# Kernel optimization log

Measured on AMD Instinct MI355X. Metric: run time of the kernel, lower is better.

The kernel has to match this reference:

```python
import jax, jax.numpy as jnp
import numpy as np

GRID_SIZE = 5
SPLINE_ORDER = 3
HIDDEN = 128
N = 131072
K = 256          # num_cluster
EPS = 1e-8       # torch.cosine_similarity eps
N_COEF = GRID_SIZE + SPLINE_ORDER  # 8 spline basis functions per input feature


def make_grid():
    # efficient-kan grid: grid_range [-1,1], extended by spline_order on each side
    h = 2.0 / GRID_SIZE
    g = jnp.arange(-SPLINE_ORDER, GRID_SIZE + SPLINE_ORDER + 1, dtype=jnp.float32) * h - 1.0
    return jnp.tile(g[None, :], (HIDDEN, 1))  # (in, grid_size + 2*order + 1) = (128, 12)


def b_splines(x, grid):
    # x: (N, in), grid: (in, G) -> bases: (N, in, grid_size + spline_order)
    xe = x[..., None]
    bases = ((xe >= grid[:, :-1]) & (xe < grid[:, 1:])).astype(x.dtype)
    for p in range(1, SPLINE_ORDER + 1):
        left = (xe - grid[:, :-(p + 1)]) / (grid[:, p:-1] - grid[:, :-(p + 1)])
        right = (grid[:, p + 1:] - xe) / (grid[:, p + 1:] - grid[:, 1:-p])
        bases = left * bases[..., :-1] + right * bases[..., 1:]
    return bases


def kan_linear(x, grid, base_w, spline_w, scaler):
    # efficient-kan KANLinear: base path + spline path
    base = jax.nn.silu(x) @ base_w.T                       # (N, out)
    sp = b_splines(x, grid)                                # (N, in, coef)
    sw = spline_w * scaler[..., None]                      # (out, in, coef)
    return base + jnp.einsum('nic,oic->no', sp, sw)


def setup_inputs() -> dict:
    key = jax.random.key(0)
    ks = jax.random.split(key, 9)
    s = 1.0 / np.sqrt(HIDDEN)
    return {
        'x': jax.random.normal(ks[0], (N, HIDDEN), jnp.float32),
        'prototypes': jax.random.normal(ks[1], (K, HIDDEN), jnp.float32),
        'grid': make_grid(),
        'base_w1': jax.random.normal(ks[2], (HIDDEN, HIDDEN), jnp.float32) * s,
        'spline_w1': jax.random.normal(ks[3], (HIDDEN, HIDDEN, N_COEF), jnp.float32) * 0.1,
        'scaler1': jax.random.normal(ks[4], (HIDDEN, HIDDEN), jnp.float32) * s + 1.0,
        'base_w2': jax.random.normal(ks[5], (HIDDEN, HIDDEN), jnp.float32) * s,
        'spline_w2': jax.random.normal(ks[6], (HIDDEN, HIDDEN, N_COEF), jnp.float32) * 0.1,
        'scaler2': jax.random.normal(ks[7], (HIDDEN, HIDDEN), jnp.float32) * s + 1.0,
    }


def reference(x, prototypes, grid, base_w1, spline_w1, scaler1, base_w2, spline_w2, scaler2):
    # KAN([128,128,128]) = two KANLinear layers
    h = kan_linear(x, grid, base_w1, spline_w1, scaler1)
    emb = kan_linear(h, grid, base_w2, spline_w2, scaler2)     # (N, 128)
    # cosine similarity to all prototypes = normalized matmul (same math as
    # the broadcasted torch.cosine_similarity, without the (N,K,H) intermediate)
    xn = emb / jnp.maximum(jnp.linalg.norm(emb, axis=-1, keepdims=True), EPS)
    pn = prototypes / jnp.maximum(jnp.linalg.norm(prototypes, axis=-1, keepdims=True), EPS)
    sim = xn @ pn.T                                            # (N, K)
    cluster_assignments = jnp.argmax(sim, axis=1)              # (N,)
    return emb, cluster_assignments
```

## Files before the change

### kernel.cpp

```cpp
#include <hip/hip_runtime.h>
#include <math.h>

typedef unsigned short u16;
typedef _Float16 f16;
typedef __attribute__((ext_vector_type(8))) _Float16 f16x8;
typedef __attribute__((ext_vector_type(2))) _Float16 f16x2;
typedef __attribute__((ext_vector_type(4))) float f32x4;

#define N_ROWS 131072
#define HID 128
#define WS_CH 8192
#define N_WCH 72
#define N_PCH 8

__device__ __forceinline__ void split8(const float* a8, f16x8& hv, f16x8& lv) {
    union { f16x8 v; f16x2 p[4]; } H, L;
    #pragma unroll
    for (int j = 0; j < 4; ++j) {
        float v0 = a8[2 * j], v1 = a8[2 * j + 1];
        float h0 = __builtin_bit_cast(float, __builtin_bit_cast(unsigned, v0) & 0xFFFFE000u);
        float h1 = __builtin_bit_cast(float, __builtin_bit_cast(unsigned, v1) & 0xFFFFE000u);
        H.p[j] = __builtin_bit_cast(f16x2, __builtin_amdgcn_cvt_pkrtz(v0, v1));
        L.p[j] = __builtin_bit_cast(f16x2, __builtin_amdgcn_cvt_pkrtz(v0 - h0, v1 - h1));
    }
    hv = H.v; lv = L.v;
}

__device__ __forceinline__ void spline8(float xv, float* a8) {
    float s  = (xv + 2.2f) * 2.5f;
    float tf = floorf(s);
    int   tt = (int)tf;
    bool valid = (tt >= 0) && (tt <= 10);
    float kt = (float)(tt - 3) * 0.4f - 1.0f;
    float u  = (xv - kt) * 2.5f;
    float u2 = u * u, u3 = u2 * u;
    float om = 1.0f - u;
    float b3 = u3 * (1.0f / 6.0f);
    float b2 = (-3.f * u3 + 3.f * u2 + 3.f * u + 1.f) * (1.0f / 6.0f);
    float b1 = (3.f * u3 - 6.f * u2 + 4.f) * (1.0f / 6.0f);
    float b0 = om * om * om * (1.0f / 6.0f);
    #pragma unroll
    for (int c = 0; c < 8; ++c) {
        int d = tt - c;
        float v = 0.f;
        v = (d == 0) ? b3 : v;
        v = (d == 1) ? b2 : v;
        v = (d == 2) ? b1 : v;
        v = (d == 3) ? b0 : v;
        a8[c] = valid ? v : 0.f;
    }
}

__device__ __forceinline__ int tswz(int r, int c) {
    return (r << 7) + ((((c >> 2) ^ r) & 31) << 2) + (c & 3);
}

__global__ __launch_bounds__(256)
void pack_weights(const float* __restrict__ bw1, const float* __restrict__ sw1,
                  const float* __restrict__ sc1,
                  const float* __restrict__ bw2, const float* __restrict__ sw2,
                  const float* __restrict__ sc2,
                  const float* __restrict__ protos, u16* __restrict__ ws)
{
    int gid = blockIdx.x * 256 + threadIdx.x;
    if (gid < N_WCH * 4096) {
        int l  = gid / (36 * 4096);
        int r  = gid % (36 * 4096);
        int ch = r / 4096;
        int e  = r % 4096;
        int o  = e >> 5;
        int kl = e & 31;
        const float* bw = l ? bw2 : bw1;
        const float* sw = l ? sw2 : sw1;
        const float* sc = l ? sc2 : sc1;
        float v;
        if (ch < 4) {
            v = bw[o * HID + ch * 32 + kl];
        } else {
            int i = (ch - 4) * 4 + (kl >> 3);
            v = sw[(o * HID + i) * 8 + (kl & 7)] * sc[o * HID + i];
        }
        f16 hi = (f16)v;
        f16 lo = (f16)(v - (float)hi);
        int nt = o >> 4, n = o & 15, kq = kl >> 3, c = kl & 7;
        size_t base = (size_t)(l * 36 + ch) * WS_CH;
        size_t idx  = ((size_t)nt * 64 + kq * 16 + n) * 8 + c;
        ws[base + idx]        = __builtin_bit_cast(u16, hi);
        ws[base + 4096 + idx] = __builtin_bit_cast(u16, lo);
    } else if (gid < (N_WCH + N_PCH) * 4096) {
        int r  = gid - N_WCH * 4096;
        int hk = r / 4096;
        int e  = r % 4096;
        int pl = e >> 5;
        int kl = e & 31;
        int half = hk >> 2, kc = hk & 3;
        int p = half * 128 + pl;
        const float4 pv = *(const float4*)(protos + (size_t)p * HID + kl * 4);
        float s = pv.x * pv.x + pv.y * pv.y + pv.z * pv.z + pv.w * pv.w;
        #pragma unroll
        for (int off = 1; off < 32; off <<= 1) s += __shfl_xor(s, off);
        float rp = 1.0f / fmaxf(sqrtf(s), 1e-8f);
        float v = protos[(size_t)p * HID + kc * 32 + kl] * rp;
        f16 hi = (f16)v;
        f16 lo = (f16)(v - (float)hi);
        int nt = pl >> 4, n = pl & 15, kq = kl >> 3, c = kl & 7;
        size_t base = (size_t)(N_WCH + hk) * WS_CH;
        size_t idx  = ((size_t)nt * 64 + kq * 16 + n) * 8 + c;
        ws[base + idx]        = __builtin_bit_cast(u16, hi);
        ws[base + 4096 + idx] = __builtin_bit_cast(u16, lo);
    }
}

__global__ __launch_bounds__(256, 3)
void kan_fused(const float* __restrict__ x, const u16* __restrict__ wpack,
               float* __restrict__ emb_out, float* __restrict__ assign_out)
{
    __shared__ float t[64 * 128];
    __shared__ u16   Bfrag[2][8][64][8];

    const int tid  = threadIdx.x;
    const int lane = tid & 63;
    const int w    = tid >> 6;
    const int m    = lane & 15;
    const int q    = lane >> 4;
    const int row  = w * 16 + m;
    const int brow = blockIdx.x * 64;

    const char* gptr = (const char*)wpack + (size_t)w * 4096 + (size_t)lane * 16;
    uint4* const lptr = (uint4*)&Bfrag[0][0][0][0] + w * 256 + lane;
    uint4 rr0, rr1, rr2, rr3;

#define ISSUE_LOADS() do {                                                         \
        rr0 = *(const uint4*)(gptr);                                               \
        rr1 = *(const uint4*)(gptr + 1024);                                        \
        rr2 = *(const uint4*)(gptr + 2048);                                        \
        rr3 = *(const uint4*)(gptr + 3072);                                        \
        gptr += 16384;                                                             \
    } while (0)

#define STORE_LDS() do {                                                           \
        lptr[0] = rr0; lptr[64] = rr1; lptr[128] = rr2; lptr[192] = rr3;           \
    } while (0)

#define PIPE_BARRIER() do {                                                        \
        asm volatile("s_waitcnt lgkmcnt(0)" ::: "memory");                         \
        __builtin_amdgcn_s_barrier();                                              \
        __builtin_amdgcn_sched_barrier(0);                                         \
    } while (0)

    ISSUE_LOADS();

    {
        const int m2 = tid >> 2, kq2 = tid & 3;
        const float4* src = (const float4*)(x + (size_t)(brow + m2) * HID + kq2 * 32);
        #pragma unroll
        for (int j = 0; j < 8; ++j) {
            float4 v = src[j];
            *(float4*)&t[tswz(m2, kq2 * 32 + j * 4)] = v;
        }
    }

    f16x8 ahv, alv, bhv, blv;
    f32x4 acc[8];

    for (int l = 0; l < 2; ++l) {
        #pragma unroll
        for (int nt = 0; nt < 8; ++nt) acc[nt] = (f32x4){0.f, 0.f, 0.f, 0.f};

        for (int ch = 0; ch < 36; ++ch) {
            float a8[8];
            if (ch < 4) {
                float4 v0 = *(const float4*)&t[tswz(row, ch * 32 + q * 8)];
                float4 v1 = *(const float4*)&t[tswz(row, ch * 32 + q * 8 + 4)];
                float xs[8] = {v0.x, v0.y, v0.z, v0.w, v1.x, v1.y, v1.z, v1.w};
                #pragma unroll
                for (int j = 0; j < 8; ++j)
                    a8[j] = xs[j] * __builtin_amdgcn_rcpf(1.0f + __expf(-xs[j]));
            } else {
                spline8(t[tswz(row, (ch - 4) * 4 + q)], a8);
            }
            split8(a8, ahv, alv);

            PIPE_BARRIER();
            STORE_LDS();
            ISSUE_LOADS();
            PIPE_BARRIER();

            __builtin_amdgcn_s_setprio(1);
            #pragma unroll
            for (int nt = 0; nt < 8; ++nt) {
                bhv = *(const f16x8*)Bfrag[0][nt][lane];
                blv = *(const f16x8*)Bfrag[1][nt][lane];
                acc[nt] = __builtin_amdgcn_mfma_f32_16x16x32_f16(ahv, bhv, acc[nt], 0, 0, 0);
                acc[nt] = __builtin_amdgcn_mfma_f32_16x16x32_f16(alv, bhv, acc[nt], 0, 0, 0);
                acc[nt] = __builtin_amdgcn_mfma_f32_16x16x32_f16(ahv, blv, acc[nt], 0, 0, 0);
            }
            __builtin_amdgcn_s_setprio(0);
        }

        #pragma unroll
        for (int nt = 0; nt < 8; ++nt)
            #pragma unroll
            for (int r = 0; r < 4; ++r)
                t[tswz(w * 16 + q * 4 + r, nt * 16 + m)] = acc[nt][r];
    }

    {
        const int m2 = tid >> 2, kq2 = tid & 3;
        float* dst = emb_out + (size_t)(brow + m2) * HID + kq2 * 32;
        #pragma unroll
        for (int j = 0; j < 8; ++j)
            *(float4*)(dst + j * 4) = *(const float4*)&t[tswz(m2, kq2 * 32 + j * 4)];
    }

    float best[4]; int bi[4];
    #pragma unroll
    for (int r = 0; r < 4; ++r) { best[r] = -3.402823466e+38f; bi[r] = 0; }

    for (int half = 0; half < 2; ++half) {
        #pragma unroll
        for (int nt = 0; nt < 8; ++nt) acc[nt] = (f32x4){0.f, 0.f, 0.f, 0.f};

        for (int kc = 0; kc < 4; ++kc) {
            const int reg = N_WCH + half * 4 + kc;

            float a8[8];
            {
                float4 v0 = *(const float4*)&t[tswz(row, kc * 32 + q * 8)];
                float4 v1 = *(const float4*)&t[tswz(row, kc * 32 + q * 8 + 4)];
                a8[0] = v0.x; a8[1] = v0.y; a8[2] = v0.z; a8[3] = v0.w;
                a8[4] = v1.x; a8[5] = v1.y; a8[6] = v1.z; a8[7] = v1.w;
            }
            split8(a8, ahv, alv);

            PIPE_BARRIER();
            STORE_LDS();
            if (reg != 79) ISSUE_LOADS();
            PIPE_BARRIER();

            __builtin_amdgcn_s_setprio(1);
            #pragma unroll
            for (int nt = 0; nt < 8; ++nt) {
                bhv = *(const f16x8*)Bfrag[0][nt][lane];
                blv = *(const f16x8*)Bfrag[1][nt][lane];
                acc[nt] = __builtin_amdgcn_mfma_f32_16x16x32_f16(ahv, bhv, acc[nt], 0, 0, 0);
                acc[nt] = __builtin_amdgcn_mfma_f32_16x16x32_f16(alv, bhv, acc[nt], 0, 0, 0);
                acc[nt] = __builtin_amdgcn_mfma_f32_16x16x32_f16(ahv, blv, acc[nt], 0, 0, 0);
            }
            __builtin_amdgcn_s_setprio(0);
        }

        #pragma unroll
        for (int nt = 0; nt < 8; ++nt) {
            int p = half * 128 + nt * 16 + m;
            #pragma unroll
            for (int r = 0; r < 4; ++r) {
                float v = acc[nt][r];
                if (v > best[r]) { best[r] = v; bi[r] = p; }
            }
        }
    }

    #pragma unroll
    for (int r = 0; r < 4; ++r) {
        #pragma unroll
        for (int off = 1; off < 16; off <<= 1) {
            float ov = __shfl_xor(best[r], off);
            int   oi = __shfl_xor(bi[r], off);
            if (ov > best[r] || (ov == best[r] && oi < bi[r])) { best[r] = ov; bi[r] = oi; }
        }
        if (m == 0)
            assign_out[(size_t)brow + w * 16 + q * 4 + r] = (float)bi[r];
    }
#undef ISSUE_LOADS
#undef STORE_LDS
#undef PIPE_BARRIER
}

extern "C" void kernel_launch(void* const* d_in, const int* in_sizes, int n_in,
                              void* d_out, int out_size, void* d_ws, size_t ws_size,
                              hipStream_t stream) {
    (void)in_sizes; (void)n_in; (void)out_size; (void)ws_size;

    const float* x      = (const float*)d_in[0];
    const float* protos = (const float*)d_in[1];
    const float* bw1 = (const float*)d_in[3];
    const float* sw1 = (const float*)d_in[4];
    const float* sc1 = (const float*)d_in[5];
    const float* bw2 = (const float*)d_in[6];
    const float* sw2 = (const float*)d_in[7];
    const float* sc2 = (const float*)d_in[8];

    float* out    = (float*)d_out;
    float* embp   = out;
    float* assign = out + (size_t)N_ROWS * HID;
    u16*   wpack  = (u16*)d_ws;

    pack_weights<<<dim3((N_WCH + N_PCH) * 4096 / 256), dim3(256), 0, stream>>>(
        bw1, sw1, sc1, bw2, sw2, sc2, protos, wpack);
    kan_fused<<<dim3(N_ROWS / 64), dim3(256), 0, stream>>>(
        x, wpack, embp, assign);
}
```

Measured before the change: 398.2 us.

## Process two 16-row M-tiles per wave to double B-fragment reuse

Each block now handles 128 rows instead of 64, and each wave computes two 16-row tiles that share the same staged B fragments from LDS. This halves the per-row cost of weight streaming, LDS B reads and barrier overhead. In exchange the block uses a larger LDS tile (64KB for t) and twice the accumulator registers, and launch bounds drop to 2 blocks per CU, so occupancy falls and latency hiding is reduced.

```diff
diff --git a/kernel.cpp b/kernel.cpp
--- a/kernel.cpp
+++ b/kernel.cpp
@@ -111,11 +111,11 @@
     }
 }
 
-__global__ __launch_bounds__(256, 3)
+__global__ __launch_bounds__(256, 2)
 void kan_fused(const float* __restrict__ x, const u16* __restrict__ wpack,
                float* __restrict__ emb_out, float* __restrict__ assign_out)
 {
-    __shared__ float t[64 * 128];
+    __shared__ float t[128 * 128];
     __shared__ u16   Bfrag[2][8][64][8];
 
     const int tid  = threadIdx.x;
@@ -123,8 +123,8 @@
     const int w    = tid >> 6;
     const int m    = lane & 15;
     const int q    = lane >> 4;
-    const int row  = w * 16 + m;
-    const int brow = blockIdx.x * 64;
+    const int row0 = w * 32 + m;
+    const int brow = blockIdx.x * 128;
 
     const char* gptr = (const char*)wpack + (size_t)w * 4096 + (size_t)lane * 16;
     uint4* const lptr = (uint4*)&Bfrag[0][0][0][0] + w * 256 + lane;
@@ -151,35 +151,45 @@
     ISSUE_LOADS();
 
     {
-        const int m2 = tid >> 2, kq2 = tid & 3;
-        const float4* src = (const float4*)(x + (size_t)(brow + m2) * HID + kq2 * 32);
-        #pragma unroll
-        for (int j = 0; j < 8; ++j) {
+        const int m2 = tid >> 1, hf = tid & 1;
+        const float4* src = (const float4*)(x + (size_t)(brow + m2) * HID + hf * 64);
+        #pragma unroll
+        for (int j = 0; j < 16; ++j) {
             float4 v = src[j];
-            *(float4*)&t[tswz(m2, kq2 * 32 + j * 4)] = v;
-        }
-    }
-
-    f16x8 ahv, alv, bhv, blv;
-    f32x4 acc[8];
+            *(float4*)&t[tswz(m2, hf * 64 + j * 4)] = v;
+        }
+    }
+
+    f16x8 ah0, al0, ah1, al1, bhv, blv;
+    f32x4 acc0[8], acc1[8];
 
     for (int l = 0; l < 2; ++l) {
         #pragma unroll
-        for (int nt = 0; nt < 8; ++nt) acc[nt] = (f32x4){0.f, 0.f, 0.f, 0.f};
+        for (int nt = 0; nt < 8; ++nt) {
+            acc0[nt] = (f32x4){0.f, 0.f, 0.f, 0.f};
+            acc1[nt] = (f32x4){0.f, 0.f, 0.f, 0.f};
+        }
 
         for (int ch = 0; ch < 36; ++ch) {
-            float a8[8];
+            float a80[8], a81[8];
             if (ch < 4) {
-                float4 v0 = *(const float4*)&t[tswz(row, ch * 32 + q * 8)];
-                float4 v1 = *(const float4*)&t[tswz(row, ch * 32 + q * 8 + 4)];
-                float xs[8] = {v0.x, v0.y, v0.z, v0.w, v1.x, v1.y, v1.z, v1.w};
+                float4 u0 = *(const float4*)&t[tswz(row0, ch * 32 + q * 8)];
+                float4 u1 = *(const float4*)&t[tswz(row0, ch * 32 + q * 8 + 4)];
+                float4 v0 = *(const float4*)&t[tswz(row0 + 16, ch * 32 + q * 8)];
+                float4 v1 = *(const float4*)&t[tswz(row0 + 16, ch * 32 + q * 8 + 4)];
+                float xs0[8] = {u0.x, u0.y, u0.z, u0.w, u1.x, u1.y, u1.z, u1.w};
+                float xs1[8] = {v0.x, v0.y, v0.z, v0.w, v1.x, v1.y, v1.z, v1.w};
                 #pragma unroll
-                for (int j = 0; j < 8; ++j)
-                    a8[j] = xs[j] * __builtin_amdgcn_rcpf(1.0f + __expf(-xs[j]));
+                for (int j = 0; j < 8; ++j) {
+                    a80[j] = xs0[j] * __builtin_amdgcn_rcpf(1.0f + __expf(-xs0[j]));
+                    a81[j] = xs1[j] * __builtin_amdgcn_rcpf(1.0f + __expf(-xs1[j]));
+                }
             } else {
-                spline8(t[tswz(row, (ch - 4) * 4 + q)], a8);
-            }
-            split8(a8, ahv, alv);
+                spline8(t[tswz(row0,      (ch - 4) * 4 + q)], a80);
+                spline8(t[tswz(row0 + 16, (ch - 4) * 4 + q)], a81);
+            }
+            split8(a80, ah0, al0);
+            split8(a81, ah1, al1);
 
             PIPE_BARRIER();
             STORE_LDS();
@@ -191,9 +201,12 @@
             for (int nt = 0; nt < 8; ++nt) {
                 bhv = *(const f16x8*)Bfrag[0][nt][lane];
                 blv = *(const f16x8*)Bfrag[1][nt][lane];
-                acc[nt] = __builtin_amdgcn_mfma_f32_16x16x32_f16(ahv, bhv, acc[nt], 0, 0, 0);
-                acc[nt] = __builtin_amdgcn_mfma_f32_16x16x32_f16(alv, bhv, acc[nt], 0, 0, 0);
-                acc[nt] = __builtin_amdgcn_mfma_f32_16x16x32_f16(ahv, blv, acc[nt], 0, 0, 0);
+                acc0[nt] = __builtin_amdgcn_mfma_f32_16x16x32_f16(ah0, bhv, acc0[nt], 0, 0, 0);
+                acc0[nt] = __builtin_amdgcn_mfma_f32_16x16x32_f16(al0, bhv, acc0[nt], 0, 0, 0);
+                acc0[nt] = __builtin_amdgcn_mfma_f32_16x16x32_f16(ah0, blv, acc0[nt], 0, 0, 0);
+                acc1[nt] = __builtin_amdgcn_mfma_f32_16x16x32_f16(ah1, bhv, acc1[nt], 0, 0, 0);
+                acc1[nt] = __builtin_amdgcn_mfma_f32_16x16x32_f16(al1, bhv, acc1[nt], 0, 0, 0);
+                acc1[nt] = __builtin_amdgcn_mfma_f32_16x16x32_f16(ah1, blv, acc1[nt], 0, 0, 0);
             }
             __builtin_amdgcn_s_setprio(0);
         }
@@ -201,37 +214,50 @@
         #pragma unroll
         for (int nt = 0; nt < 8; ++nt)
             #pragma unroll
-            for (int r = 0; r < 4; ++r)
-                t[tswz(w * 16 + q * 4 + r, nt * 16 + m)] = acc[nt][r];
+            for (int r = 0; r < 4; ++r) {
+                t[tswz(w * 32 + q * 4 + r,      nt * 16 + m)] = acc0[nt][r];
+                t[tswz(w * 32 + 16 + q * 4 + r, nt * 16 + m)] = acc1[nt][r];
+            }
     }
 
     {
-        const int m2 = tid >> 2, kq2 = tid & 3;
-        float* dst = emb_out + (size_t)(brow + m2) * HID + kq2 * 32;
-        #pragma unroll
-        for (int j = 0; j < 8; ++j)
-            *(float4*)(dst + j * 4) = *(const float4*)&t[tswz(m2, kq2 * 32 + j * 4)];
-    }
-
-    float best[4]; int bi[4];
+        const int m2 = tid >> 1, hf = tid & 1;
+        float* dst = emb_out + (size_t)(brow + m2) * HID + hf * 64;
+        #pragma unroll
+        for (int j = 0; j < 16; ++j)
+            *(float4*)(dst + j * 4) = *(const float4*)&t[tswz(m2, hf * 64 + j * 4)];
+    }
+
+    float best0[4], best1[4]; int bi0[4], bi1[4];
     #pragma unroll
-    for (int r = 0; r < 4; ++r) { best[r] = -3.402823466e+38f; bi[r] = 0; }
+    for (int r = 0; r < 4; ++r) {
+        best0[r] = -3.402823466e+38f; bi0[r] = 0;
+        best1[r] = -3.402823466e+38f; bi1[r] = 0;
+    }
 
     for (int half = 0; half < 2; ++half) {
         #pragma unroll
-        for (int nt = 0; nt < 8; ++nt) acc[nt] = (f32x4){0.f, 0.f, 0.f, 0.f};
+        for (int nt = 0; nt < 8; ++nt) {
+            acc0[nt] = (f32x4){0.f, 0.f, 0.f, 0.f};
+            acc1[nt] = (f32x4){0.f, 0.f, 0.f, 0.f};
+        }
 
         for (int kc = 0; kc < 4; ++kc) {
             const int reg = N_WCH + half * 4 + kc;
 
-            float a8[8];
+            float a80[8], a81[8];
             {
-                float4 v0 = *(const float4*)&t[tswz(row, kc * 32 + q * 8)];
-                float4 v1 = *(const float4*)&t[tswz(row, kc * 32 + q * 8 + 4)];
-                a8[0] = v0.x; a8[1] = v0.y; a8[2] = v0.z; a8[3] = v0.w;
-                a8[4] = v1.x; a8[5] = v1.y; a8[6] = v1.z; a8[7] = v1.w;
-            }
-            split8(a8, ahv, alv);
+                float4 u0 = *(const float4*)&t[tswz(row0, kc * 32 + q * 8)];
+                float4 u1 = *(const float4*)&t[tswz(row0, kc * 32 + q * 8 + 4)];
+                float4 v0 = *(const float4*)&t[tswz(row0 + 16, kc * 32 + q * 8)];
+                float4 v1 = *(const float4*)&t[tswz(row0 + 16, kc * 32 + q * 8 + 4)];
+                a80[0] = u0.x; a80[1] = u0.y; a80[2] = u0.z; a80[3] = u0.w;
+                a80[4] = u1.x; a80[5] = u1.y; a80[6] = u1.z; a80[7] = u1.w;
+                a81[0] = v0.x; a81[1] = v0.y; a81[2] = v0.z; a81[3] = v0.w;
+                a81[4] = v1.x; a81[5] = v1.y; a81[6] = v1.z; a81[7] = v1.w;
+            }
+            split8(a80, ah0, al0);
+            split8(a81, ah1, al1);
 
             PIPE_BARRIER();
             STORE_LDS();
@@ -243,9 +269,12 @@
             for (int nt = 0; nt < 8; ++nt) {
                 bhv = *(const f16x8*)Bfrag[0][nt][lane];
                 blv = *(const f16x8*)Bfrag[1][nt][lane];
-                acc[nt] = __builtin_amdgcn_mfma_f32_16x16x32_f16(ahv, bhv, acc[nt], 0, 0, 0);
-                acc[nt] = __builtin_amdgcn_mfma_f32_16x16x32_f16(alv, bhv, acc[nt], 0, 0, 0);
-                acc[nt] = __builtin_amdgcn_mfma_f32_16x16x32_f16(ahv, blv, acc[nt], 0, 0, 0);
+                acc0[nt] = __builtin_amdgcn_mfma_f32_16x16x32_f16(ah0, bhv, acc0[nt], 0, 0, 0);
+                acc0[nt] = __builtin_amdgcn_mfma_f32_16x16x32_f16(al0, bhv, acc0[nt], 0, 0, 0);
+                acc0[nt] = __builtin_amdgcn_mfma_f32_16x16x32_f16(ah0, blv, acc0[nt], 0, 0, 0);
+                acc1[nt] = __builtin_amdgcn_mfma_f32_16x16x32_f16(ah1, bhv, acc1[nt], 0, 0, 0);
+                acc1[nt] = __builtin_amdgcn_mfma_f32_16x16x32_f16(al1, bhv, acc1[nt], 0, 0, 0);
+                acc1[nt] = __builtin_amdgcn_mfma_f32_16x16x32_f16(ah1, blv, acc1[nt], 0, 0, 0);
             }
             __builtin_amdgcn_s_setprio(0);
         }
@@ -255,8 +284,10 @@
             int p = half * 128 + nt * 16 + m;
             #pragma unroll
             for (int r = 0; r < 4; ++r) {
-                float v = acc[nt][r];
-                if (v > best[r]) { best[r] = v; bi[r] = p; }
+                float v0 = acc0[nt][r];
+                if (v0 > best0[r]) { best0[r] = v0; bi0[r] = p; }
+                float v1 = acc1[nt][r];
+                if (v1 > best1[r]) { best1[r] = v1; bi1[r] = p; }
             }
         }
     }
@@ -265,12 +296,17 @@
     for (int r = 0; r < 4; ++r) {
         #pragma unroll
         for (int off = 1; off < 16; off <<= 1) {
-            float ov = __shfl_xor(best[r], off);
-            int   oi = __shfl_xor(bi[r], off);
-            if (ov > best[r] || (ov == best[r] && oi < bi[r])) { best[r] = ov; bi[r] = oi; }
-        }
-        if (m == 0)
-            assign_out[(size_t)brow + w * 16 + q * 4 + r] = (float)bi[r];
+            float ov0 = __shfl_xor(best0[r], off);
+            int   oi0 = __shfl_xor(bi0[r], off);
+            if (ov0 > best0[r] || (ov0 == best0[r] && oi0 < bi0[r])) { best0[r] = ov0; bi0[r] = oi0; }
+            float ov1 = __shfl_xor(best1[r], off);
+            int   oi1 = __shfl_xor(bi1[r], off);
+            if (ov1 > best1[r] || (ov1 == best1[r] && oi1 < bi1[r])) { best1[r] = ov1; bi1[r] = oi1; }
+        }
+        if (m == 0) {
+            assign_out[(size_t)brow + w * 32 + q * 4 + r]      = (float)bi0[r];
+            assign_out[(size_t)brow + w * 32 + 16 + q * 4 + r] = (float)bi1[r];
+        }
     }
 #undef ISSUE_LOADS
 #undef STORE_LDS
@@ -298,6 +334,6 @@
 
     pack_weights<<<dim3((N_WCH + N_PCH) * 4096 / 256), dim3(256), 0, stream>>>(
         bw1, sw1, sc1, bw2, sw2, sc2, protos, wpack);
-    kan_fused<<<dim3(N_ROWS / 64), dim3(256), 0, stream>>>(
+    kan_fused<<<dim3(N_ROWS / 128), dim3(256), 0, stream>>>(
         x, wpack, embp, assign);
 }
```

Result: faster. 388.9 us (-2.3%).
